# Kernel tuning notes

Measured on AMD Instinct MI355X. Metric: run time of the kernel, lower is better.

Reference implementation:

```python
import jax, jax.numpy as jnp
import numpy as np

RHO = 0.5
MASK = 1.0
FR0 = 4096  # ifft length along fast-time axis
FR1 = 512   # fft length along slow-time (Doppler) axis
WIN = 8     # sliding-window length of the phase-reference accumulator
EPS_DENOM = 1e-6


def setup_inputs() -> dict:
    key = jax.random.key(0)
    k1, k2 = jax.random.split(key)
    x_real = jax.random.normal(k1, (8, 4096, 256), dtype=jnp.float32)
    x_imag = jax.random.normal(k2, (8, 4096, 256), dtype=jnp.float32)
    return {"x_real": x_real, "x_imag": x_imag}


def _phase_com_doppler(inp):
    # inp: [B, N, M_in] complex; ifft along last axis padded/truncated to FR0
    final = jnp.fft.ifft(inp, n=FR0, axis=2)  # [B, N, M]
    B, N, M = final.shape
    out0 = final[:, 0, :]                      # [B, M]
    # reproduces the torch `if k < 7` branch without control flow.
    buf0 = jnp.zeros((WIN, B, M), final.dtype).at[WIN - 1].set(out0)

    def step(carry, f_k1):
        pref, buf = carry
        s = jnp.sum(jnp.conj(pref) * f_k1, axis=-1, keepdims=True)  # [B,1]
        phase = s / jnp.abs(s)
        o = f_k1 * jnp.conj(phase)                                  # [B,M]
        pref = pref + o - buf[0]
        buf = jnp.concatenate([buf[1:], o[None]], axis=0)
        return (pref, buf), o

    seq = jnp.swapaxes(final, 0, 1)[1:]        # [N-1, B, M]
    _, outs = jax.lax.scan(step, (out0, buf0), seq)
    out = jnp.concatenate([out0[None], outs], axis=0)  # [N, B, M]
    out = jnp.swapaxes(out, 0, 1)              # [B, N, M]
    # fft along pulse axis padded to FR1
    return jnp.fft.fft(out, n=FR1, axis=1)     # [B, FR1, M]


def reference(x_real, x_imag):
    x = jax.lax.complex(x_real, x_imag)        # [B, P, Q] complex64
    denom = MASK + RHO
    denom = EPS_DENOM if denom == 0 else denom
    x2 = x * (1.0 / denom)
    out3 = _phase_com_doppler(jnp.swapaxes(x2, -1, -2))  # [B, FR1, FR0]
    out3 = jnp.swapaxes(out3, -1, -2)          # [B, FR0, FR1]
    # cs_data dict -> tuple ('input', 'nnline_input')
    return (x, out3)
```

## Files before the change

kernel.cpp:

```cpp
#include <hip/hip_runtime.h>
#include <math.h>

#define NF 4096
#define NC 256
#define NJ 512
#define CH 128
#define TWO_PI_F 6.28318530717958647692f

__device__ __forceinline__ float2 cmul(float2 a, float2 b) {
    return make_float2(a.x*b.x - a.y*b.y, a.x*b.y + a.y*b.x);
}

__device__ __forceinline__ void dft4i(float2& x0, float2& x1, float2& x2, float2& x3, float sgn) {
    float2 t0 = make_float2(x0.x + x2.x, x0.y + x2.y);
    float2 t1 = make_float2(x0.x - x2.x, x0.y - x2.y);
    float2 t2 = make_float2(x1.x + x3.x, x1.y + x3.y);
    float2 t3 = make_float2(x1.x - x3.x, x1.y - x3.y);
    float2 it3 = make_float2(-sgn * t3.y, sgn * t3.x);
    x0 = make_float2(t0.x + t2.x, t0.y + t2.y);
    x2 = make_float2(t0.x - t2.x, t0.y - t2.y);
    x1 = make_float2(t1.x + it3.x, t1.y + it3.y);
    x3 = make_float2(t1.x - it3.x, t1.y - it3.y);
}

__device__ __forceinline__ void dft16(float2* u, float sgn) {
    dft4i(u[0], u[4], u[8],  u[12], sgn);
    dft4i(u[1], u[5], u[9],  u[13], sgn);
    dft4i(u[2], u[6], u[10], u[14], sgn);
    dft4i(u[3], u[7], u[11], u[15], sgn);
    const float C1 = 0.9238795325112867f, S1 = 0.3826834323650898f, R2 = 0.7071067811865476f;
    u[5]  = cmul(u[5],  make_float2(C1,  sgn * S1));
    u[6]  = cmul(u[6],  make_float2(R2,  sgn * R2));
    u[7]  = cmul(u[7],  make_float2(S1,  sgn * C1));
    u[9]  = cmul(u[9],  make_float2(R2,  sgn * R2));
    u[10] = cmul(u[10], make_float2(0.f, sgn));
    u[11] = cmul(u[11], make_float2(-R2, sgn * R2));
    u[13] = cmul(u[13], make_float2(S1,  sgn * C1));
    u[14] = cmul(u[14], make_float2(-R2, sgn * R2));
    u[15] = cmul(u[15], make_float2(-C1, -sgn * S1));
    dft4i(u[0],  u[1],  u[2],  u[3],  sgn);
    dft4i(u[4],  u[5],  u[6],  u[7],  sgn);
    dft4i(u[8],  u[9],  u[10], u[11], sgn);
    dft4i(u[12], u[13], u[14], u[15], sgn);
}

__device__ __forceinline__ void dft8(const float2* u, float2* v, float sgn) {
    float2 e0 = u[0], e1 = u[2], e2 = u[4], e3 = u[6];
    float2 o0 = u[1], o1 = u[3], o2 = u[5], o3 = u[7];
    dft4i(e0, e1, e2, e3, sgn);
    dft4i(o0, o1, o2, o3, sgn);
    const float R2 = 0.7071067811865476f;
    float2 w1 = make_float2(R2, sgn * R2);
    float2 w2 = make_float2(0.f, sgn);
    float2 w3 = make_float2(-R2, sgn * R2);
    float2 t1 = cmul(o1, w1), t2 = cmul(o2, w2), t3 = cmul(o3, w3);
    v[0] = make_float2(e0.x + o0.x, e0.y + o0.y);
    v[4] = make_float2(e0.x - o0.x, e0.y - o0.y);
    v[1] = make_float2(e1.x + t1.x, e1.y + t1.y);
    v[5] = make_float2(e1.x - t1.x, e1.y - t1.y);
    v[2] = make_float2(e2.x + t2.x, e2.y + t2.y);
    v[6] = make_float2(e2.x - t2.x, e2.y - t2.y);
    v[3] = make_float2(e3.x + t3.x, e3.y + t3.y);
    v[7] = make_float2(e3.x - t3.x, e3.y - t3.y);
}

__global__ __launch_bounds__(256) void transpose_kernel(const float* __restrict__ xr,
                                                        const float* __restrict__ xi,
                                                        float2* __restrict__ fin,
                                                        int b0, int nbm1, int nbshift) {
    __shared__ float ldr[64][65];
    __shared__ float ldi[64][65];
    int wg = blockIdx.x;
    int bl = wg & nbm1;
    int rest = wg >> nbshift;
    int ft = rest & 63;
    int ct = rest >> 6;
    int f0 = ft << 6, c0 = ct << 6;
    int t = threadIdx.x;
    int cl = t & 63;
    int rq = t >> 6;
    const float scale = 1.0f / (4096.0f * 1.5f);
    int bg = b0 + bl;
    const float* xrb = xr + (size_t)bg * NF * NC;
    const float* xib = xi + (size_t)bg * NF * NC;
#pragma unroll
    for (int q = 0; q < 16; q++) {
        int r = q * 4 + rq;
        size_t idx = (size_t)(f0 + r) * NC + c0 + cl;
        ldr[cl][r] = xrb[idx] * scale;
        ldi[cl][r] = xib[idx] * scale;
    }
    __syncthreads();
    int fl = t & 63;
#pragma unroll
    for (int q = 0; q < 16; q++) {
        int cr = q * 4 + rq;
        fin[((size_t)(bl * NC + c0 + cr)) * NF + f0 + fl] =
            make_float2(ldr[cr][fl], ldi[cr][fl]);
    }
}

#define IPAD(a) ((a) + ((a) >> 4))

template<int P>
__device__ __forceinline__ void pass16(float2* S, int t, float sgn) {
    const int k = t & (P - 1);
    float2 u[16];
#pragma unroll
    for (int r = 0; r < 16; r++) u[r] = S[IPAD(t + 256 * r)];
    __syncthreads();
    if (P > 1) {
        float ab = sgn * (TWO_PI_F / (16.0f * (float)P)) * (float)k;
#pragma unroll
        for (int r = 1; r < 16; r++) {
            float sn, cs; __sincosf(ab * (float)r, &sn, &cs);
            u[r] = cmul(u[r], make_float2(cs, sn));
        }
    }
    dft16(u, sgn);
    const int base = 16 * P * (t / P) + k;
#pragma unroll
    for (int j = 0; j < 16; j++) {
        const int sl = ((j & 3) << 2) | (j >> 2);
        S[IPAD(base + j * P)] = u[sl];
    }
    __syncthreads();
}

__global__ __launch_bounds__(256) void ifft4096_kernel(float2* __restrict__ fin,
                                                       int bmask, int bshift) {
    __shared__ float2 S[4352];
    int wg = blockIdx.x;
    int bl = wg & bmask;
    int c = wg >> bshift;
    int t = threadIdx.x;
    size_t base = ((size_t)(bl * NC + c)) * NF;
#pragma unroll
    for (int q = 0; q < 16; q++) {
        int f = t + 256 * q;
        S[IPAD(f)] = fin[base + f];
    }
    __syncthreads();
    pass16<1>(S, t, 1.0f);
    pass16<16>(S, t, 1.0f);
    pass16<256>(S, t, 1.0f);
#pragma unroll
    for (int q = 0; q < 16; q++) {
        int f = t + 256 * q;
        fin[base + f] = S[IPAD(f)];
    }
}

__global__ __launch_bounds__(256) void gram_kernel(const float2* __restrict__ fin,
                                                   float2* __restrict__ gpart) {
    __shared__ float2 ring[16][CH];
    int wg = blockIdx.x;
    int bl = wg >> 7;
    int ch = (wg >> 2) & 31;
    int ks = wg & 3;
    int m0 = ch * CH;
    int k0 = ks * 64;
    int kend = k0 + 64;
    int t = threadIdx.x;
    int dgrp = t >> 5;
    int lane = t & 31;
    for (int r = (k0 >= 8 ? k0 - 8 : 0); r <= k0; r++)
        if (t < CH) ring[r & 15][t] = fin[((size_t)(bl * NC + r)) * NF + m0 + t];
    __syncthreads();
    for (int k = k0; k < kend; k++) {
        float2 nxt;
        bool ld = (k + 1 < kend) && (t < CH);
        if (ld) nxt = fin[((size_t)(bl * NC + k + 1)) * NF + m0 + t];
        int d = dgrp + 1;
        float2 acc = make_float2(0.f, 0.f);
        if (k - d >= 0) {
            int sk = k & 15, sj = (k - d) & 15;
#pragma unroll
            for (int i = 0; i < 4; i++) {
                int m = lane + 32 * i;
                float2 a = ring[sj][m];
                float2 bb = ring[sk][m];
                acc.x += a.x * bb.x + a.y * bb.y;
                acc.y += a.x * bb.y - a.y * bb.x;
            }
        }
#pragma unroll
        for (int off = 16; off >= 1; off >>= 1) {
            acc.x += __shfl_xor(acc.x, off);
            acc.y += __shfl_xor(acc.y, off);
        }
        if (lane == 0)
            gpart[((size_t)(bl * 32 + ch) * NC + k) * 8 + dgrp] = acc;
        if (ld) ring[(k + 1) & 15][t] = nxt;
        __syncthreads();
    }
}

__global__ void gsum_kernel(const float2* __restrict__ gpart, float2* __restrict__ gs, int total) {
    int e = blockIdx.x * blockDim.x + threadIdx.x;
    if (e >= total) return;
    int bl = e >> 11;
    int kd = e & 2047;
    float2 s = make_float2(0.f, 0.f);
    for (int ch = 0; ch < 32; ch++) {
        float2 v = gpart[((size_t)(bl * 32 + ch)) * 2048 + kd];
        s.x += v.x; s.y += v.y;
    }
    gs[e] = s;
}

#define SCAN_STEP(A0, A1, A2, A3, KIDX)  do {                                  \
    float rx0 = p1.x*A0.x - p1.y*A0.y, ry0 = p1.x*A0.y + p1.y*A0.x;            \
    float rx1 = p2.x*A0.z - p2.y*A0.w, ry1 = p2.x*A0.w + p2.y*A0.z;            \
    float rx2 = p3.x*A1.x - p3.y*A1.y, ry2 = p3.x*A1.y + p3.y*A1.x;            \
    float rx3 = p4.x*A1.z - p4.y*A1.w, ry3 = p4.x*A1.w + p4.y*A1.z;            \
    float rx4 = p5.x*A2.x - p5.y*A2.y, ry4 = p5.x*A2.y + p5.y*A2.x;            \
    float rx5 = p6.x*A2.z - p6.y*A2.w, ry5 = p6.x*A2.w + p6.y*A2.z;            \
    float rx6 = p7.x*A3.x - p7.y*A3.y, ry6 = p7.x*A3.y + p7.y*A3.x;            \
    float rx7 = p8.x*A3.z - p8.y*A3.w, ry7 = p8.x*A3.w + p8.y*A3.z;            \
    float sx = ((rx0 + rx1) + (rx2 + rx3)) + ((rx4 + rx5) + (rx6 + rx7));      \
    float sy = ((ry0 + ry1) + (ry2 + ry3)) + ((ry4 + ry5) + (ry6 + ry7));      \
    float inv = 1.0f / sqrtf(sx * sx + sy * sy);                               \
    float2 np = make_float2(sx * inv, sy * inv);                               \
    phase[t * NC + (KIDX)] = np;                                               \
    p8 = p7; p7 = p6; p6 = p5; p5 = p4; p4 = p3; p3 = p2; p2 = p1; p1 = np;    \
} while (0)

#define SCAN_LOADG(BUF, KBASE)  do {                                           \
    _Pragma("unroll") for (int j = 0; j < 8; j++) {                            \
        _Pragma("unroll") for (int q = 0; q < 4; q++)                          \
            BUF[j][q] = gb4[((KBASE) + j) * 4 + q];                            \
    }                                                                          \
} while (0)

#define SCAN_GRP(BUF, KBASE, FIRST)  do {                                      \
    _Pragma("unroll") for (int j = 0; j < 8; j++) {                            \
        if (FIRST && j == 0) {                                                 \
            phase[t * NC] = make_float2(1.f, 0.f);                             \
        } else {                                                               \
            SCAN_STEP(BUF[j][0], BUF[j][1], BUF[j][2], BUF[j][3], (KBASE) + j);\
        }                                                                      \
    }                                                                          \
} while (0)

__global__ __launch_bounds__(64) void scan_kernel(const float2* __restrict__ gs,
                                                  float2* __restrict__ phase, int nb) {
    int t = threadIdx.x;
    if (t >= nb) return;
    const float4* gb4 = (const float4*)(gs + (size_t)t * 2048);
    float2 z = make_float2(0.f, 0.f);
    float2 p1 = make_float2(1.f, 0.f);
    float2 p2 = z, p3 = z, p4 = z, p5 = z, p6 = z, p7 = z, p8 = z;
    float4 GA[8][4], GB[8][4];
    SCAN_LOADG(GA, 0);
    for (int g2 = 0; g2 < 16; g2++) {
        int k0 = g2 * 16;
        SCAN_LOADG(GB, k0 + 8);
        if (g2 == 0) { SCAN_GRP(GA, k0, true); } else { SCAN_GRP(GA, k0, false); }
        if (g2 < 15) SCAN_LOADG(GA, k0 + 16);
        SCAN_GRP(GB, k0 + 8, false);
    }
}

__global__ void scale_kernel(float4* __restrict__ fin4, const float2* __restrict__ phase, int n4) {
    int i = blockIdx.x * blockDim.x + threadIdx.x;
    if (i >= n4) return;
    int row = i >> 11;
    float2 ph = phase[row];
    float4 v = fin4[i];
    fin4[i] = make_float4(v.x*ph.x + v.y*ph.y, v.y*ph.x - v.x*ph.y,
                          v.z*ph.x + v.w*ph.y, v.w*ph.x - v.z*ph.y);
}

#define FPAD 516

template<int P, bool ZTOP>
__device__ __forceinline__ void pass8x(float2* L, int fp, int i2, float sgn) {
    const int ia = i2, ib = i2 + 32;
    const int ka = ia & (P - 1), kb = ib & (P - 1);
    float2 ua[8], ub[8];
#pragma unroll
    for (int r = 0; r < 8; r++) {
        if (ZTOP && r >= 4) {
            ua[r] = make_float2(0.f, 0.f);
            ub[r] = make_float2(0.f, 0.f);
        } else {
            ua[r] = L[fp * FPAD + ia + 64 * r];
            ub[r] = L[fp * FPAD + ib + 64 * r];
        }
    }
    __syncthreads();
    if (P > 1) {
        float aba = sgn * (TWO_PI_F / (8.0f * (float)P)) * (float)ka;
        float abb = sgn * (TWO_PI_F / (8.0f * (float)P)) * (float)kb;
#pragma unroll
        for (int r = 1; r < 8; r++) {
            float sn, cs;
            __sincosf(aba * (float)r, &sn, &cs);
            ua[r] = cmul(ua[r], make_float2(cs, sn));
            __sincosf(abb * (float)r, &sn, &cs);
            ub[r] = cmul(ub[r], make_float2(cs, sn));
        }
    }
    float2 va[8], vb[8];
    dft8(ua, va, sgn);
    dft8(ub, vb, sgn);
    const int basea = 8 * P * (ia / P) + ka;
    const int baseb = 8 * P * (ib / P) + kb;
#pragma unroll
    for (int r = 0; r < 8; r++) {
        L[fp * FPAD + basea + r * P] = va[r];
        L[fp * FPAD + baseb + r * P] = vb[r];
    }
    __syncthreads();
}

__global__ __launch_bounds__(256) void fft512_kernel(const float2* __restrict__ fin,
                                                     const float2* __restrict__ ph,
                                                     float* __restrict__ outr,
                                                     float2* __restrict__ outc,
                                                     int b0, int realOnly) {
    __shared__ float2 L[8 * FPAD];
    int wg = blockIdx.x;
    int bl = wg >> 9;
    int f0 = (wg & 511) * 8;
    int t = threadIdx.x;
    int fpp = t & 7;
    int cg = t >> 3;
#pragma unroll
    for (int it = 0; it < 8; it++) {
        int c = it * 32 + cg;
        float2 v = fin[((size_t)(bl * NC + c)) * NF + f0 + fpp];
        if (ph) {
            float2 p = ph[bl * NC + c];
            v = make_float2(v.x * p.x + v.y * p.y, v.y * p.x - v.x * p.y);
        }
        L[fpp * FPAD + c] = v;
    }
    __syncthreads();
    int fp = t & 7;
    int i2 = t >> 3;
    pass8x<1, true >(L, fp, i2, -1.0f);
    pass8x<8, false>(L, fp, i2, -1.0f);
    pass8x<64, false>(L, fp, i2, -1.0f);
    size_t ob = ((size_t)((b0 + bl) * NF + f0)) * NJ;
    if (realOnly) {
#pragma unroll
        for (int fp2 = 0; fp2 < 8; fp2++)
#pragma unroll
            for (int jq = 0; jq < 2; jq++) {
                int j = t + 256 * jq;
                outr[ob + (size_t)fp2 * NJ + j] = L[fp2 * FPAD + j].x;
            }
    } else {
#pragma unroll
        for (int fp2 = 0; fp2 < 8; fp2++)
#pragma unroll
            for (int jq = 0; jq < 2; jq++) {
                int j = t + 256 * jq;
                outc[ob + (size_t)fp2 * NJ + j] = L[fp2 * FPAD + j];
            }
    }
}

__global__ void copy_kernel(const float4* __restrict__ src, float4* __restrict__ dst, int n4) {
    int i = blockIdx.x * blockDim.x + threadIdx.x;
    int stride = gridDim.x * blockDim.x;
    for (; i < n4; i += stride) dst[i] = src[i];
}
__global__ void pack_x_kernel(const float2* __restrict__ xr, const float2* __restrict__ xi,
                              float4* __restrict__ out, int n4) {
    int i = blockIdx.x * blockDim.x + threadIdx.x;
    int stride = gridDim.x * blockDim.x;
    for (; i < n4; i += stride) {
        float2 r = xr[i], m = xi[i];
        out[i] = make_float4(r.x, m.x, r.y, m.y);
    }
}

extern "C" void kernel_launch(void* const* d_in, const int* in_sizes, int n_in,
                              void* d_out, int out_size, void* d_ws, size_t ws_size,
                              hipStream_t stream) {
    const float* xr = (const float*)d_in[0];
    const float* xi = (const float*)d_in[1];
    float* out = (float*)d_out;

    if (out_size < 40000000) {
        float* out0r = out;
        float* out3r = out + 8388608;
        size_t need = (size_t)(8388608 + 524288 + 16384 + 2048) * sizeof(float2);
        if (ws_size >= need) {
            float2* fin   = (float2*)d_ws;
            float2* gpart = fin + 8388608;
            float2* gsb   = gpart + 524288;
            float2* phase = gsb + 16384;
            transpose_kernel<<<8 * 256, 256, 0, stream>>>(xr, xi, fin, 0, 7, 3);
            ifft4096_kernel<<<8 * NC, 256, 0, stream>>>(fin, 7, 3);
            gram_kernel<<<8 * 128, 256, 0, stream>>>(fin, gpart);
            gsum_kernel<<<(8 * 2048) / 256, 256, 0, stream>>>(gpart, gsb, 8 * 2048);
            scan_kernel<<<1, 64, 0, stream>>>(gsb, phase, 8);
            fft512_kernel<<<8 * 512, 256, 0, stream>>>(fin, phase, out3r, nullptr, 0, 1);
        } else {
            float2* fin   = (float2*)out0r;
            float2* o3f2  = (float2*)out3r;
            float2* gpart = o3f2 + (8388608 - 262144 - 8192 - 1024);
            float2* gsb   = o3f2 + (8388608 - 8192 - 1024);
            float2* phase = o3f2 + (8388608 - 1024);
            for (int p = 0; p < 2; p++) {
                int b0 = p * 4;
                transpose_kernel<<<4 * 256, 256, 0, stream>>>(xr, xi, fin, b0, 3, 2);
                ifft4096_kernel<<<4 * NC, 256, 0, stream>>>(fin, 3, 2);
                gram_kernel<<<4 * 128, 256, 0, stream>>>(fin, gpart);
                gsum_kernel<<<(4 * 2048) / 256, 256, 0, stream>>>(gpart, gsb, 4 * 2048);
                scan_kernel<<<1, 64, 0, stream>>>(gsb, phase, 4);
                scale_kernel<<<4 * 2048, 256, 0, stream>>>((float4*)fin, phase, 4 * 524288);
                fft512_kernel<<<4 * 512, 256, 0, stream>>>(fin, nullptr, out3r, nullptr, b0, 1);
            }
        }
        copy_kernel<<<2048, 256, 0, stream>>>((const float4*)xr, (float4*)out0r, 2097152);
    } else {
        float2* out0f2 = (float2*)out;
        float2* out3f2 = (float2*)(out + 16777216);
        float2* fin   = out0f2;
        float2* gpart = out3f2 + (16777216 - 524288 - 16384 - 2048);
        float2* gsb   = out3f2 + (16777216 - 16384 - 2048);
        float2* phase = out3f2 + (16777216 - 2048);
        transpose_kernel<<<8 * 256, 256, 0, stream>>>(xr, xi, fin, 0, 7, 3);
        ifft4096_kernel<<<8 * NC, 256, 0, stream>>>(fin, 7, 3);
        gram_kernel<<<8 * 128, 256, 0, stream>>>(fin, gpart);
        gsum_kernel<<<(8 * 2048) / 256, 256, 0, stream>>>(gpart, gsb, 8 * 2048);
        scan_kernel<<<1, 64, 0, stream>>>(gsb, phase, 8);
        scale_kernel<<<8 * 2048, 256, 0, stream>>>((float4*)fin, phase, 8 * 524288);
        fft512_kernel<<<8 * 512, 256, 0, stream>>>(fin, nullptr, nullptr, out3f2, 0, 0);
        pack_x_kernel<<<4096, 256, 0, stream>>>((const float2*)xr, (const float2*)xi,
                                                (float4*)out0f2, 4194304);
    }
}
```

Before: 210.2 us.

## Overlap input copy with serial phase scan in one fused launch

```diff
diff --git a/kernel.cpp b/kernel.cpp
--- a/kernel.cpp
+++ b/kernel.cpp
@@ -220,21 +220,21 @@
     float rx7 = p8.x*A3.z - p8.y*A3.w, ry7 = p8.x*A3.w + p8.y*A3.z;            \
     float sx = ((rx0 + rx1) + (rx2 + rx3)) + ((rx4 + rx5) + (rx6 + rx7));      \
     float sy = ((ry0 + ry1) + (ry2 + ry3)) + ((ry4 + ry5) + (ry6 + ry7));      \
-    float inv = 1.0f / sqrtf(sx * sx + sy * sy);                               \
+    float inv = rsqrtf(sx * sx + sy * sy);                                     \
     float2 np = make_float2(sx * inv, sy * inv);                               \
     phase[t * NC + (KIDX)] = np;                                               \
     p8 = p7; p7 = p6; p6 = p5; p5 = p4; p4 = p3; p3 = p2; p2 = p1; p1 = np;    \
 } while (0)
 
-#define SCAN_LOADG(BUF, KBASE)  do {                                           \
-    _Pragma("unroll") for (int j = 0; j < 8; j++) {                            \
+#define SCAN_LOADG4(BUF, KBASE)  do {                                          \
+    _Pragma("unroll") for (int j = 0; j < 4; j++) {                            \
         _Pragma("unroll") for (int q = 0; q < 4; q++)                          \
             BUF[j][q] = gb4[((KBASE) + j) * 4 + q];                            \
     }                                                                          \
 } while (0)
 
-#define SCAN_GRP(BUF, KBASE, FIRST)  do {                                      \
-    _Pragma("unroll") for (int j = 0; j < 8; j++) {                            \
+#define SCAN_GRP4(BUF, KBASE, FIRST)  do {                                     \
+    _Pragma("unroll") for (int j = 0; j < 4; j++) {                            \
         if (FIRST && j == 0) {                                                 \
             phase[t * NC] = make_float2(1.f, 0.f);                             \
         } else {                                                               \
@@ -243,22 +243,32 @@
     }                                                                          \
 } while (0)
 
-__global__ __launch_bounds__(64) void scan_kernel(const float2* __restrict__ gs,
-                                                  float2* __restrict__ phase, int nb) {
+__global__ __launch_bounds__(64, 1) void scan_copy_kernel(const float2* __restrict__ gs,
+                                                          float2* __restrict__ phase, int nb,
+                                                          const float4* __restrict__ csrc,
+                                                          float4* __restrict__ cdst, int cn4) {
+    if (blockIdx.x != 0) {
+        int i = (blockIdx.x - 1) * 64 + threadIdx.x;
+        int stride = (gridDim.x - 1) * 64;
+        for (; i < cn4; i += stride) cdst[i] = csrc[i];
+        return;
+    }
     int t = threadIdx.x;
     if (t >= nb) return;
     const float4* gb4 = (const float4*)(gs + (size_t)t * 2048);
     float2 z = make_float2(0.f, 0.f);
     float2 p1 = make_float2(1.f, 0.f);
     float2 p2 = z, p3 = z, p4 = z, p5 = z, p6 = z, p7 = z, p8 = z;
-    float4 GA[8][4], GB[8][4];
-    SCAN_LOADG(GA, 0);
-    for (int g2 = 0; g2 < 16; g2++) {
-        int k0 = g2 * 16;
-        SCAN_LOADG(GB, k0 + 8);
-        if (g2 == 0) { SCAN_GRP(GA, k0, true); } else { SCAN_GRP(GA, k0, false); }
-        if (g2 < 15) SCAN_LOADG(GA, k0 + 16);
-        SCAN_GRP(GB, k0 + 8, false);
+    float4 GA[4][4], GB[4][4];
+    SCAN_LOADG4(GA, 0);
+    for (int g2 = 0; g2 < 32; g2++) {
+        int k0 = g2 * 8;
+        SCAN_LOADG4(GB, k0 + 4);
+        __builtin_amdgcn_sched_barrier(0);
+        if (g2 == 0) { SCAN_GRP4(GA, k0, true); } else { SCAN_GRP4(GA, k0, false); }
+        if (g2 < 31) SCAN_LOADG4(GA, k0 + 8);
+        __builtin_amdgcn_sched_barrier(0);
+        SCAN_GRP4(GB, k0 + 4, false);
     }
 }
 
@@ -398,7 +408,8 @@
             ifft4096_kernel<<<8 * NC, 256, 0, stream>>>(fin, 7, 3);
             gram_kernel<<<8 * 128, 256, 0, stream>>>(fin, gpart);
             gsum_kernel<<<(8 * 2048) / 256, 256, 0, stream>>>(gpart, gsb, 8 * 2048);
-            scan_kernel<<<1, 64, 0, stream>>>(gsb, phase, 8);
+            scan_copy_kernel<<<2049, 64, 0, stream>>>(gsb, phase, 8,
+                                                      (const float4*)xr, (float4*)out0r, 2097152);
             fft512_kernel<<<8 * 512, 256, 0, stream>>>(fin, phase, out3r, nullptr, 0, 1);
         } else {
             float2* fin   = (float2*)out0r;
@@ -412,12 +423,12 @@
                 ifft4096_kernel<<<4 * NC, 256, 0, stream>>>(fin, 3, 2);
                 gram_kernel<<<4 * 128, 256, 0, stream>>>(fin, gpart);
                 gsum_kernel<<<(4 * 2048) / 256, 256, 0, stream>>>(gpart, gsb, 4 * 2048);
-                scan_kernel<<<1, 64, 0, stream>>>(gsb, phase, 4);
+                scan_copy_kernel<<<1, 64, 0, stream>>>(gsb, phase, 4, nullptr, nullptr, 0);
                 scale_kernel<<<4 * 2048, 256, 0, stream>>>((float4*)fin, phase, 4 * 524288);
                 fft512_kernel<<<4 * 512, 256, 0, stream>>>(fin, nullptr, out3r, nullptr, b0, 1);
             }
-        }
-        copy_kernel<<<2048, 256, 0, stream>>>((const float4*)xr, (float4*)out0r, 2097152);
+            copy_kernel<<<2048, 256, 0, stream>>>((const float4*)xr, (float4*)out0r, 2097152);
+        }
     } else {
         float2* out0f2 = (float2*)out;
         float2* out3f2 = (float2*)(out + 16777216);
@@ -429,7 +440,7 @@
         ifft4096_kernel<<<8 * NC, 256, 0, stream>>>(fin, 7, 3);
         gram_kernel<<<8 * 128, 256, 0, stream>>>(fin, gpart);
         gsum_kernel<<<(8 * 2048) / 256, 256, 0, stream>>>(gpart, gsb, 8 * 2048);
-        scan_kernel<<<1, 64, 0, stream>>>(gsb, phase, 8);
+        scan_copy_kernel<<<1, 64, 0, stream>>>(gsb, phase, 8, nullptr, nullptr, 0);
         scale_kernel<<<8 * 2048, 256, 0, stream>>>((float4*)fin, phase, 8 * 524288);
         fft512_kernel<<<8 * 512, 256, 0, stream>>>(fin, nullptr, nullptr, out3f2, 0, 0);
         pack_x_kernel<<<4096, 256, 0, stream>>>((const float2*)xr, (const float2*)xi,
```

Result: faster. 188.4 us (-10.4%).
